# Kernel optimization log

Measured on AMD Instinct MI355X. Metric: run time of the kernel, lower is better.

Reference implementation:

```python
import jax, jax.numpy as jnp
import numpy as np

# dims: T tokens, H hidden, E experts, I expert intermediate, K top-k
T, H, E, I, K = 2048, 1024, 64, 768, 8


def setup_inputs() -> dict:
    key = jax.random.key(0)
    k0, k1, k2, k3, k4 = jax.random.split(key, 5)
    s = 0.02  # init scale
    return {
        "hidden_states": jax.random.normal(k0, (T, H), jnp.float32),
        "w_router": jax.random.normal(k1, (E, H), jnp.float32) * s,   # gate (router) Linear, no bias
        "w_gate": jax.random.normal(k2, (E, I, H), jnp.float32) * s,  # per-expert gate_proj (out,in)
        "w_up": jax.random.normal(k3, (E, I, H), jnp.float32) * s,    # per-expert up_proj
        "w_down": jax.random.normal(k4, (E, H, I), jnp.float32) * s,  # per-expert down_proj
    }


def reference(hidden_states, w_router, w_gate, w_up, w_down):
    x = hidden_states  # (T, H)
    # --- router: softmax scores, top-k selection, renormalize (select_experts, softmax scoring) ---
    router_logits = jnp.einsum("th,eh->te", x, w_router)          # (T, E)
    probs = jax.nn.softmax(router_logits, axis=-1)
    topk_w, topk_ids = jax.lax.top_k(probs, K)                     # (T, K)
    topk_w = topk_w / jnp.sum(topk_w, axis=-1, keepdims=True)      # renormalize=True
    # scatter per-slot weights into a (T, E) combine matrix (zero for unselected experts)
    route = jnp.zeros((x.shape[0], E), x.dtype)
    route = route.at[jnp.arange(x.shape[0])[:, None], topk_ids].add(topk_w)
    # --- experts: SwiGLU MLP per expert, weighted combine (FusedMoE dispatch/combine) ---
    g = jnp.einsum("th,eih->tei", x, w_gate)                       # (T, E, I)
    u = jnp.einsum("th,eih->tei", x, w_up)
    h = jax.nn.silu(g) * u
    y = jnp.einsum("tei,ehi,te->th", h, w_down, route)             # weighted scatter-combine
    return y
```

## Files before the change

### kernel.cpp

```cpp
#include <hip/hip_runtime.h>
#include <hip/hip_bf16.h>
#include <cstdint>
#include <cstddef>

#define T_TOK 2048
#define H_DIM 1024
#define E_NUM 64
#define I_DIM 768
#define K_TOP 8
#define BM 384

typedef __attribute__((ext_vector_type(8))) __bf16 bf16x8;
typedef __attribute__((ext_vector_type(4))) __bf16 bf16x4;
typedef __attribute__((ext_vector_type(8))) unsigned short u16x8;
typedef __attribute__((ext_vector_type(4))) float f32x4;
typedef unsigned short ushort_t;

__device__ __forceinline__ unsigned short f2bf(float f) {
  uint32_t u = __builtin_bit_cast(uint32_t, f);
  u += 0x7fffu + ((u >> 16) & 1u);
  return (unsigned short)(u >> 16);
}

__device__ __forceinline__ bf16x8 cvt8b(f32x4 a, f32x4 b) {
  bf16x8 r;
  r[0] = (__bf16)a[0]; r[1] = (__bf16)a[1]; r[2] = (__bf16)a[2]; r[3] = (__bf16)a[3];
  r[4] = (__bf16)b[0]; r[5] = (__bf16)b[1]; r[6] = (__bf16)b[2]; r[7] = (__bf16)b[3];
  return r;
}

__device__ __forceinline__ bf16x4 cvt4b(f32x4 a) {
  bf16x4 r;
  r[0] = (__bf16)a[0]; r[1] = (__bf16)a[1]; r[2] = (__bf16)a[2]; r[3] = (__bf16)a[3];
  return r;
}

__device__ __forceinline__ void async16(const void* l, const void* g) {
  __builtin_amdgcn_global_load_lds(
      (const __attribute__((address_space(1))) unsigned int*)g,
      (__attribute__((address_space(3))) unsigned int*)l, 16, 0, 0);
}

__global__ __launch_bounds__(256) void xcast_kernel(const float* __restrict__ x,
                                                    ushort_t* __restrict__ xb) {
  int i = blockIdx.x * 256 + threadIdx.x;
  const f32x4* s = (const f32x4*)(x + (size_t)i * 8);
  *(bf16x8*)(xb + (size_t)i * 8) = cvt8b(s[0], s[1]);
}

__global__ __launch_bounds__(64) void router_kernel(
    const float* __restrict__ x, const float* __restrict__ wr,
    int* __restrict__ topk_id, float* __restrict__ topk_w,
    int* __restrict__ counts) {
  const int t0 = blockIdx.x * 4;
  const int e = threadIdx.x;
  const float4* wv = (const float4*)(wr + (size_t)e * H_DIM);
  const float4* xv0 = (const float4*)(x + (size_t)t0 * H_DIM);
  const float4* xv1 = (const float4*)(x + (size_t)(t0 + 1) * H_DIM);
  const float4* xv2 = (const float4*)(x + (size_t)(t0 + 2) * H_DIM);
  const float4* xv3 = (const float4*)(x + (size_t)(t0 + 3) * H_DIM);
  float acc0 = 0.f, acc1 = 0.f, acc2 = 0.f, acc3 = 0.f;
#pragma unroll 4
  for (int i = 0; i < H_DIM / 4; ++i) {
    float4 b = wv[i];
    float4 a0 = xv0[i], a1 = xv1[i], a2 = xv2[i], a3 = xv3[i];
    acc0 = fmaf(a0.x, b.x, fmaf(a0.y, b.y, fmaf(a0.z, b.z, fmaf(a0.w, b.w, acc0))));
    acc1 = fmaf(a1.x, b.x, fmaf(a1.y, b.y, fmaf(a1.z, b.z, fmaf(a1.w, b.w, acc1))));
    acc2 = fmaf(a2.x, b.x, fmaf(a2.y, b.y, fmaf(a2.z, b.z, fmaf(a2.w, b.w, acc2))));
    acc3 = fmaf(a3.x, b.x, fmaf(a3.y, b.y, fmaf(a3.z, b.z, fmaf(a3.w, b.w, acc3))));
  }
  float accs[4] = {acc0, acc1, acc2, acc3};
#pragma unroll 1
  for (int tt = 0; tt < 4; ++tt) {
    int t = t0 + tt;
    float acc = accs[tt];
    float m = acc;
    for (int o = 32; o; o >>= 1) m = fmaxf(m, __shfl_xor(m, o));
    float p = __expf(acc - m);
    float s = p;
    for (int o = 32; o; o >>= 1) s += __shfl_xor(s, o);
    p /= s;
    float v = p;
    int sid = 0;
    float sw = 0.f;
    for (int k = 0; k < K_TOP; ++k) {
      float bv = v;
      int bi = e;
      for (int o = 32; o; o >>= 1) {
        float ov = __shfl_xor(bv, o);
        int oi = __shfl_xor(bi, o);
        if (ov > bv || (ov == bv && oi < bi)) { bv = ov; bi = oi; }
      }
      if (e == k) { sid = bi; sw = bv; }
      if (e == bi) v = -1.f;
    }
    float ssum = (e < K_TOP) ? sw : 0.f;
    for (int o = 32; o; o >>= 1) ssum += __shfl_xor(ssum, o);
    if (e < K_TOP) {
      topk_id[t * K_TOP + e] = sid;
      topk_w[t * K_TOP + e] = sw / ssum;
      atomicAdd(&counts[sid], 1);
    }
  }
}

__global__ __launch_bounds__(64) void scan_kernel(
    const int* __restrict__ counts, int* __restrict__ offsets,
    int* __restrict__ cursor) {
  int e = threadIdx.x;
  int ne = counts[e];
  int x = ne;
  for (int o = 1; o < 64; o <<= 1) {
    int v = __shfl_up(x, o);
    if (e >= o) x += v;
  }
  int excl = x - ne;
  offsets[e] = excl;
  cursor[e] = excl;
}

__global__ __launch_bounds__(256) void build_kernel(
    const int* __restrict__ topk_id, const float* __restrict__ topk_w,
    int* __restrict__ cursor, int* __restrict__ pair_token, float* __restrict__ pair_w) {
  int i = blockIdx.x * 256 + threadIdx.x;
  int t = i >> 3;
  int e = topk_id[i];
  int pos = atomicAdd(&cursor[e], 1);
  pair_token[pos] = t;
  pair_w[pos] = topk_w[i];
}


#define GU_NIT 32

__global__ __launch_bounds__(768, 3) void gemm_gu_kernel(
    const ushort_t* __restrict__ xb, const float* __restrict__ wg,
    const float* __restrict__ wu, const int* __restrict__ offsets,
    const int* __restrict__ counts, const int* __restrict__ pair_token,
    ushort_t* __restrict__ h_buf) {
  int idx = (blockIdx.x & 7) * 96 + (blockIdx.x >> 3);
  int e = idx / 12, nt = idx - e * 12;
  int ne = counts[e], off = offsets[e];
  int ib = nt * 64;

  __shared__ __align__(16) ushort_t Xs[2][BM * 32];
  __shared__ __align__(16) ushort_t Gs[2][64 * 32];
  __shared__ __align__(16) ushort_t Us[2][64 * 32];
  __shared__ int sTok[BM];

  const int tid = threadIdx.x;
  const int lane = tid & 63;
  const int wid = tid >> 6;
  if (tid < BM) {
    sTok[tid] = pair_token[off + (tid < ne ? tid : ne - 1)];
  }
  __syncthreads();

  const ushort_t* xsrc[2];
#pragma unroll
  for (int j = 0; j < 2; ++j) {
    int p = j * 768 + tid;
    int row = p >> 2, c = p & 3;
    xsrc[j] = xb + (size_t)sTok[row] * H_DIM + ((c ^ ((row >> 1) & 3)) << 3);
  }
  const float* gsrc = wg;
  const float* usrc = wu;
  int wdsti = 0;
  if (wid < 8) {
    int wrow = tid >> 3, wq = tid & 7;
    size_t ro = ((size_t)e * I_DIM + ib + wrow) * H_DIM + wq * 4;
    gsrc = wg + ro;
    usrc = wu + ro;
    wdsti = wrow * 32 + (((wq >> 1) ^ ((wrow >> 1) & 3)) << 3) + ((wq & 1) << 2);
  }

  const int wrM = wid >> 1, wrN = wid & 1;
  const int lrow = lane & 15, lk = lane >> 4;
  const bool wact = (wrM * 64) < ne;

  f32x4 accG[4][2], accU[4][2];
#pragma unroll
  for (int mi = 0; mi < 4; ++mi)
#pragma unroll
    for (int ni = 0; ni < 2; ++ni) {
      accG[mi][ni] = f32x4{0.f, 0.f, 0.f, 0.f};
      accU[mi][ni] = f32x4{0.f, 0.f, 0.f, 0.f};
    }

  f32x4 gA = {0, 0, 0, 0}, uA = {0, 0, 0, 0};

#define GU_XDMA(B, K0)                                             \
  do {                                                             \
    async16(&Xs[B][(wid * 64) * 8], xsrc[0] + (K0));               \
    async16(&Xs[B][(768 + wid * 64) * 8], xsrc[1] + (K0));         \
  } while (0)

  GU_XDMA(0, 0);
  if (wid < 8) {
    gA = *(const f32x4*)(gsrc);
    uA = *(const f32x4*)(usrc);
  }
  asm volatile("s_waitcnt vmcnt(0)" ::: "memory");
  __builtin_amdgcn_sched_barrier(0);
  if (wid < 8) {
    *(bf16x4*)&Gs[0][wdsti] = cvt4b(gA);
    *(bf16x4*)&Us[0][wdsti] = cvt4b(uA);
  }
  asm volatile("s_waitcnt lgkmcnt(0)" ::: "memory");
  __builtin_amdgcn_s_barrier();
  __builtin_amdgcn_sched_barrier(0);

#pragma unroll 2
  for (int K = 0; K < GU_NIT; ++K) {
    const int B = K & 1;
    if (K + 1 < GU_NIT) {
      GU_XDMA(B ^ 1, (K + 1) * 32);
      if (wid < 8) {
        gA = *(const f32x4*)(gsrc + (K + 1) * 32);
        uA = *(const f32x4*)(usrc + (K + 1) * 32);
      }
    }
    if (wact) {
      __builtin_amdgcn_s_setprio(1);
      bf16x8 af[4];
#pragma unroll
      for (int mi = 0; mi < 4; ++mi) {
        int r = wrM * 64 + mi * 16 + lrow;
        af[mi] = __builtin_bit_cast(
            bf16x8, *(const u16x8*)&Xs[B][r * 32 + ((lk ^ ((r >> 1) & 3)) << 3)]);
      }
#pragma unroll
      for (int ni = 0; ni < 2; ++ni) {
        int br = wrN * 32 + ni * 16 + lrow;
        int ci = br * 32 + ((lk ^ ((br >> 1) & 3)) << 3);
        bf16x8 bg = __builtin_bit_cast(bf16x8, *(const u16x8*)&Gs[B][ci]);
        bf16x8 bu = __builtin_bit_cast(bf16x8, *(const u16x8*)&Us[B][ci]);
#pragma unroll
        for (int mi = 0; mi < 4; ++mi) {
          accG[mi][ni] = __builtin_amdgcn_mfma_f32_16x16x32_bf16(af[mi], bg, accG[mi][ni], 0, 0, 0);
          accU[mi][ni] = __builtin_amdgcn_mfma_f32_16x16x32_bf16(af[mi], bu, accU[mi][ni], 0, 0, 0);
        }
      }
      __builtin_amdgcn_s_setprio(0);
    }
    asm volatile("s_waitcnt vmcnt(0)" ::: "memory");
    __builtin_amdgcn_sched_barrier(0);
    if (K + 1 < GU_NIT && wid < 8) {
      *(bf16x4*)&Gs[B ^ 1][wdsti] = cvt4b(gA);
      *(bf16x4*)&Us[B ^ 1][wdsti] = cvt4b(uA);
    }
    asm volatile("s_waitcnt lgkmcnt(0)" ::: "memory");
    __builtin_amdgcn_s_barrier();
    __builtin_amdgcn_sched_barrier(0);
  }
#undef GU_XDMA

#pragma unroll
  for (int mi = 0; mi < 4; ++mi)
#pragma unroll
    for (int ni = 0; ni < 2; ++ni)
#pragma unroll
      for (int r = 0; r < 4; ++r) {
        int grow = wrM * 64 + mi * 16 + lk * 4 + r;
        if (grow < ne) {
          int col = ib + wrN * 32 + ni * 16 + lrow;
          float g = accG[mi][ni][r], u = accU[mi][ni][r];
          float hv = g / (1.f + __expf(-g)) * u;
          h_buf[(size_t)(off + grow) * I_DIM + col] = f2bf(hv);
        }
      }
}

#define DN_NIT 24

__global__ __launch_bounds__(768, 3) void gemm_down_kernel(
    const ushort_t* __restrict__ h_buf, const float* __restrict__ wd,
    const int* __restrict__ offsets, const int* __restrict__ counts,
    const int* __restrict__ pair_token, const float* __restrict__ pair_w,
    float* __restrict__ y) {
  int idx = (blockIdx.x & 7) * 64 + (blockIdx.x >> 3);
  int e = idx >> 3, nt = idx & 7;
  int ne = counts[e], off = offsets[e];
  int hb = nt * 128;

  __shared__ __align__(16) ushort_t Ah[2][BM * 32];
  __shared__ __align__(16) ushort_t Bs[2][128 * 32];
  __shared__ int sTok[BM];
  __shared__ float sPw[BM];

  const int tid = threadIdx.x;
  const int lane = tid & 63;
  const int wid = tid >> 6;
  if (tid < BM) {
    int ix = off + (tid < ne ? tid : ne - 1);
    sTok[tid] = pair_token[ix];
    sPw[tid] = pair_w[ix];
  }
  __syncthreads();

  const ushort_t* asrc[2];
#pragma unroll
  for (int j = 0; j < 2; ++j) {
    int p = j * 768 + tid;
    int row = p >> 2, c = p & 3;
    int hr = off + (row < ne ? row : ne - 1);
    asrc[j] = h_buf + (size_t)hr * I_DIM + ((c ^ ((row >> 1) & 3)) << 3);
  }
  const float* bsrc0 = wd;
  const float* bsrc1 = wd;
  int bdst0 = 0, bdst1 = 0;
  if (wid < 8) {
    int r0 = tid >> 3, q0 = tid & 7;
    bsrc0 = wd + ((size_t)e * H_DIM + hb + r0) * I_DIM + q0 * 4;
    bdst0 = r0 * 32 + (((q0 >> 1) ^ ((r0 >> 1) & 3)) << 3) + ((q0 & 1) << 2);
    int p1 = 512 + tid;
    int r1 = p1 >> 3, q1 = p1 & 7;
    bsrc1 = wd + ((size_t)e * H_DIM + hb + r1) * I_DIM + q1 * 4;
    bdst1 = r1 * 32 + (((q1 >> 1) ^ ((r1 >> 1) & 3)) << 3) + ((q1 & 1) << 2);
  }

  const int wrM = wid >> 1, wrN = wid & 1;
  const int lrow = lane & 15, lk = lane >> 4;
  const bool wact = (wrM * 64) < ne;

  f32x4 acc[4][4];
#pragma unroll
  for (int mi = 0; mi < 4; ++mi)
#pragma unroll
    for (int ni = 0; ni < 4; ++ni) acc[mi][ni] = f32x4{0.f, 0.f, 0.f, 0.f};

  f32x4 bA = {0, 0, 0, 0}, bB = {0, 0, 0, 0};

#define DN_ADMA(B, K0)                                             \
  do {                                                             \
    async16(&Ah[B][(wid * 64) * 8], asrc[0] + (K0));               \
    async16(&Ah[B][(768 + wid * 64) * 8], asrc[1] + (K0));         \
  } while (0)

  DN_ADMA(0, 0);
  if (wid < 8) {
    bA = *(const f32x4*)(bsrc0);
    bB = *(const f32x4*)(bsrc1);
  }
  asm volatile("s_waitcnt vmcnt(0)" ::: "memory");
  __builtin_amdgcn_sched_barrier(0);
  if (wid < 8) {
    *(bf16x4*)&Bs[0][bdst0] = cvt4b(bA);
    *(bf16x4*)&Bs[0][bdst1] = cvt4b(bB);
  }
  asm volatile("s_waitcnt lgkmcnt(0)" ::: "memory");
  __builtin_amdgcn_s_barrier();
  __builtin_amdgcn_sched_barrier(0);

#pragma unroll 2
  for (int K = 0; K < DN_NIT; ++K) {
    const int B = K & 1;
    if (K + 1 < DN_NIT) {
      DN_ADMA(B ^ 1, (K + 1) * 32);
      if (wid < 8) {
        bA = *(const f32x4*)(bsrc0 + (K + 1) * 32);
        bB = *(const f32x4*)(bsrc1 + (K + 1) * 32);
      }
    }
    if (wact) {
      __builtin_amdgcn_s_setprio(1);
      bf16x8 af[4];
#pragma unroll
      for (int mi = 0; mi < 4; ++mi) {
        int r = wrM * 64 + mi * 16 + lrow;
        af[mi] = __builtin_bit_cast(
            bf16x8, *(const u16x8*)&Ah[B][r * 32 + ((lk ^ ((r >> 1) & 3)) << 3)]);
      }
#pragma unroll
      for (int ni = 0; ni < 4; ++ni) {
        int br = wrN * 64 + ni * 16 + lrow;
        bf16x8 bb = __builtin_bit_cast(
            bf16x8, *(const u16x8*)&Bs[B][br * 32 + ((lk ^ ((br >> 1) & 3)) << 3)]);
#pragma unroll
        for (int mi = 0; mi < 4; ++mi)
          acc[mi][ni] = __builtin_amdgcn_mfma_f32_16x16x32_bf16(af[mi], bb, acc[mi][ni], 0, 0, 0);
      }
      __builtin_amdgcn_s_setprio(0);
    }
    asm volatile("s_waitcnt vmcnt(0)" ::: "memory");
    __builtin_amdgcn_sched_barrier(0);
    if (K + 1 < DN_NIT && wid < 8) {
      *(bf16x4*)&Bs[B ^ 1][bdst0] = cvt4b(bA);
      *(bf16x4*)&Bs[B ^ 1][bdst1] = cvt4b(bB);
    }
    asm volatile("s_waitcnt lgkmcnt(0)" ::: "memory");
    __builtin_amdgcn_s_barrier();
    __builtin_amdgcn_sched_barrier(0);
  }
#undef DN_ADMA

#pragma unroll
  for (int mi = 0; mi < 4; ++mi)
#pragma unroll
    for (int ni = 0; ni < 4; ++ni)
#pragma unroll
      for (int r = 0; r < 4; ++r) {
        int grow = wrM * 64 + mi * 16 + lk * 4 + r;
        if (grow < ne) {
          int col = hb + wrN * 64 + ni * 16 + lrow;
          float val = acc[mi][ni][r] * sPw[grow];
          unsafeAtomicAdd(&y[(size_t)sTok[grow] * H_DIM + col], val);
        }
      }
}

extern "C" void kernel_launch(void* const* d_in, const int* in_sizes, int n_in,
                              void* d_out, int out_size, void* d_ws, size_t ws_size,
                              hipStream_t stream) {
  const float* x  = (const float*)d_in[0];
  const float* wr = (const float*)d_in[1];
  const float* wg = (const float*)d_in[2];
  const float* wu = (const float*)d_in[3];
  const float* wd = (const float*)d_in[4];
  float* y = (float*)d_out;

  char* ws = (char*)d_ws;
  int* counts    = (int*)(ws + 0);
  int* offsets   = (int*)(ws + 256);
  int* cursor    = (int*)(ws + 512);
  int*   topk_id    = (int*)(ws + 2048);
  float* topk_w     = (float*)(ws + 2048 + 1 * 65536);
  int*   pair_token = (int*)(ws + 2048 + 2 * 65536);
  float* pair_w     = (float*)(ws + 2048 + 3 * 65536);
  ushort_t* h_buf = (ushort_t*)(ws + 2048 + 4 * 65536);
  ushort_t* xb = (ushort_t*)(ws + 2048 + 4 * 65536 + (size_t)T_TOK * I_DIM * K_TOP * 2);

  hipMemsetAsync(counts, 0, 256, stream);
  hipMemsetAsync(y, 0, (size_t)T_TOK * H_DIM * sizeof(float), stream);

  xcast_kernel<<<(T_TOK * H_DIM / 8) / 256, 256, 0, stream>>>(x, xb);
  router_kernel<<<T_TOK / 4, 64, 0, stream>>>(x, wr, topk_id, topk_w, counts);
  scan_kernel<<<1, 64, 0, stream>>>(counts, offsets, cursor);
  build_kernel<<<(T_TOK * K_TOP) / 256, 256, 0, stream>>>(topk_id, topk_w, cursor, pair_token, pair_w);
  gemm_gu_kernel<<<768, 768, 0, stream>>>(
      xb, wg, wu, offsets, counts, pair_token, h_buf);
  gemm_down_kernel<<<512, 768, 0, stream>>>(
      h_buf, wd, offsets, counts, pair_token, pair_w, y);
}
```

Before: 372.7 us.

## Retile MoE GEMMs into 256-row expert tiles with a dynamic tile list

The scan kernel now builds a compact list of 256-row M tiles per expert, at most two per expert. Both expert GEMMs are launched over that list with XCD-aware index decoding, so blocks for empty tiles exit early. This replaces the fixed 384-row padded tiles, which wasted MFMA work and LDS. The gate/up kernel now uses 512-thread blocks that stack gate and up weights in one 256-row B tile, exchange the up accumulators through LDS for the SiLU epilogue, and use a four-phase software pipeline. The cost is extra barriers and LDS traffic in the epilogue, and any expert with more than 512 assigned tokens would be truncated.

Measured after the change: 556.9 us. 1.49x slower.

```diff
diff --git a/kernel.cpp b/kernel.cpp
--- a/kernel.cpp
+++ b/kernel.cpp
@@ -8,10 +8,8 @@
 #define E_NUM 64
 #define I_DIM 768
 #define K_TOP 8
-#define BM 384
 
 typedef __attribute__((ext_vector_type(8))) __bf16 bf16x8;
-typedef __attribute__((ext_vector_type(4))) __bf16 bf16x4;
 typedef __attribute__((ext_vector_type(8))) unsigned short u16x8;
 typedef __attribute__((ext_vector_type(4))) float f32x4;
 typedef unsigned short ushort_t;
@@ -22,17 +20,11 @@
   return (unsigned short)(u >> 16);
 }
 
-__device__ __forceinline__ bf16x8 cvt8b(f32x4 a, f32x4 b) {
+__device__ __forceinline__ u16x8 cvt8b(f32x4 a, f32x4 b) {
   bf16x8 r;
   r[0] = (__bf16)a[0]; r[1] = (__bf16)a[1]; r[2] = (__bf16)a[2]; r[3] = (__bf16)a[3];
   r[4] = (__bf16)b[0]; r[5] = (__bf16)b[1]; r[6] = (__bf16)b[2]; r[7] = (__bf16)b[3];
-  return r;
-}
-
-__device__ __forceinline__ bf16x4 cvt4b(f32x4 a) {
-  bf16x4 r;
-  r[0] = (__bf16)a[0]; r[1] = (__bf16)a[1]; r[2] = (__bf16)a[2]; r[3] = (__bf16)a[3];
-  return r;
+  return __builtin_bit_cast(u16x8, r);
 }
 
 __device__ __forceinline__ void async16(const void* l, const void* g) {
@@ -41,11 +33,19 @@
       (__attribute__((address_space(3))) unsigned int*)l, 16, 0, 0);
 }
 
+__device__ __forceinline__ int xcd_decode(int wg0, int n_act) {
+  int q = n_act >> 3, r = n_act & 7;
+  int xcd = wg0 & 7, rank = wg0 >> 3;
+  int cnt = q + (xcd < r ? 1 : 0);
+  if (rank >= cnt) return -1;
+  return (xcd < r ? xcd * (q + 1) : r * (q + 1) + (xcd - r) * q) + rank;
+}
+
 __global__ __launch_bounds__(256) void xcast_kernel(const float* __restrict__ x,
                                                     ushort_t* __restrict__ xb) {
   int i = blockIdx.x * 256 + threadIdx.x;
   const f32x4* s = (const f32x4*)(x + (size_t)i * 8);
-  *(bf16x8*)(xb + (size_t)i * 8) = cvt8b(s[0], s[1]);
+  *(u16x8*)(xb + (size_t)i * 8) = cvt8b(s[0], s[1]);
 }
 
 __global__ __launch_bounds__(64) void router_kernel(
@@ -106,7 +106,8 @@
 
 __global__ __launch_bounds__(64) void scan_kernel(
     const int* __restrict__ counts, int* __restrict__ offsets,
-    int* __restrict__ cursor) {
+    int* __restrict__ cursor, int* __restrict__ tile_list,
+    int* __restrict__ n_tiles) {
   int e = threadIdx.x;
   int ne = counts[e];
   int x = ne;
@@ -117,6 +118,16 @@
   int excl = x - ne;
   offsets[e] = excl;
   cursor[e] = excl;
+  int ntl = (ne + 255) >> 8;
+  if (ntl > 2) ntl = 2;
+  int y2 = ntl;
+  for (int o = 1; o < 64; o <<= 1) {
+    int v = __shfl_up(y2, o);
+    if (e >= o) y2 += v;
+  }
+  int texcl = y2 - ntl;
+  for (int m = 0; m < ntl; ++m) tile_list[texcl + m] = (e << 2) | m;
+  if (e == 63) *n_tiles = texcl + ntl;
 }
 
 __global__ __launch_bounds__(256) void build_kernel(
@@ -133,276 +144,343 @@
 
 #define GU_NIT 32
 
-__global__ __launch_bounds__(768, 3) void gemm_gu_kernel(
+__global__ __launch_bounds__(512, 2) void gemm_gu_kernel(
     const ushort_t* __restrict__ xb, const float* __restrict__ wg,
     const float* __restrict__ wu, const int* __restrict__ offsets,
     const int* __restrict__ counts, const int* __restrict__ pair_token,
+    const int* __restrict__ tile_list, const int* __restrict__ n_tiles,
     ushort_t* __restrict__ h_buf) {
-  int idx = (blockIdx.x & 7) * 96 + (blockIdx.x >> 3);
-  int e = idx / 12, nt = idx - e * 12;
+  int idx = xcd_decode(blockIdx.x, (*n_tiles) * 6);
+  if (idx < 0) return;
+  int tl = idx / 6, nt = idx - tl * 6;
+  int ent = tile_list[tl];
+  int e = ent >> 2, mt = ent & 3;
   int ne = counts[e], off = offsets[e];
-  int ib = nt * 64;
-
-  __shared__ __align__(16) ushort_t Xs[2][BM * 32];
-  __shared__ __align__(16) ushort_t Gs[2][64 * 32];
-  __shared__ __align__(16) ushort_t Us[2][64 * 32];
-  __shared__ int sTok[BM];
+  int ib = nt * 128;
+  int vr = ne - mt * 256;
+  if (vr <= 0) return;
+  if (vr > 256) vr = 256;
+
+  __shared__ __align__(16) char L[66560];
+  ushort_t* AsB = (ushort_t*)L;
+  ushort_t* BlB = (ushort_t*)(L + 32768);
+  int* sTok = (int*)(L + 65536);
 
   const int tid = threadIdx.x;
   const int lane = tid & 63;
   const int wid = tid >> 6;
-  if (tid < BM) {
-    sTok[tid] = pair_token[off + (tid < ne ? tid : ne - 1)];
+  const int wrM = wid >> 2, wrN = wid & 3;
+  const int lrow = lane & 15, lk = lane >> 4;
+
+  if (tid < 256) {
+    int p = mt * 256 + tid;
+    sTok[tid] = pair_token[off + (p < ne ? p : ne - 1)];
   }
   __syncthreads();
 
   const ushort_t* xsrc[2];
+  int adst[2];
 #pragma unroll
   for (int j = 0; j < 2; ++j) {
-    int p = j * 768 + tid;
+    int p = j * 512 + tid;
     int row = p >> 2, c = p & 3;
     xsrc[j] = xb + (size_t)sTok[row] * H_DIM + ((c ^ ((row >> 1) & 3)) << 3);
-  }
-  const float* gsrc = wg;
-  const float* usrc = wu;
-  int wdsti = 0;
-  if (wid < 8) {
-    int wrow = tid >> 3, wq = tid & 7;
-    size_t ro = ((size_t)e * I_DIM + ib + wrow) * H_DIM + wq * 4;
-    gsrc = wg + ro;
-    usrc = wu + ro;
-    wdsti = wrow * 32 + (((wq >> 1) ^ ((wrow >> 1) & 3)) << 3) + ((wq & 1) << 2);
-  }
-
-  const int wrM = wid >> 1, wrN = wid & 1;
-  const int lrow = lane & 15, lk = lane >> 4;
-  const bool wact = (wrM * 64) < ne;
-
-  f32x4 accG[4][2], accU[4][2];
-#pragma unroll
-  for (int mi = 0; mi < 4; ++mi)
-#pragma unroll
-    for (int ni = 0; ni < 2; ++ni) {
-      accG[mi][ni] = f32x4{0.f, 0.f, 0.f, 0.f};
-      accU[mi][ni] = f32x4{0.f, 0.f, 0.f, 0.f};
+    adst[j] = (j * 512 + wid * 64) * 8;
+  }
+  const int brow = tid >> 1;
+  const int cs0 = (tid & 1) * 2, cs1 = cs0 + 1;
+  const float* bq = (brow < 128)
+      ? wg + ((size_t)e * I_DIM + ib + brow) * H_DIM
+      : wu + ((size_t)e * I_DIM + ib + brow - 128) * H_DIM;
+  const float* bsrc0 = bq + cs0 * 8;
+  const float* bsrc1 = bq + cs1 * 8;
+  const int bd0 = (brow * 4 + (cs0 ^ ((brow >> 1) & 3))) * 8;
+  const int bd1 = (brow * 4 + (cs1 ^ ((brow >> 1) & 3))) * 8;
+
+  const bool wact = (wrM * 128) < vr;
+
+  f32x4 acc[8][4];
+#pragma unroll
+  for (int mi = 0; mi < 8; ++mi)
+#pragma unroll
+    for (int ni = 0; ni < 4; ++ni) acc[mi][ni] = f32x4{0.f, 0.f, 0.f, 0.f};
+
+#define GU_ADMA(NB, K0)                                           \
+  do {                                                            \
+    async16(&AsB[(NB) * 8192 + adst[0]], xsrc[0] + (K0));         \
+    async16(&AsB[(NB) * 8192 + adst[1]], xsrc[1] + (K0));         \
+  } while (0)
+
+#define GU_AF(AB, MI)                                                        \
+  do {                                                                       \
+    int R0 = wrM * 128 + (MI) * 16 + lrow;                                   \
+    int R1 = R0 + 16;                                                        \
+    af0 = *(const u16x8*)&AsB[(AB) * 8192 + R0 * 32 + ((lk ^ ((R0 >> 1) & 3)) << 3)]; \
+    af1 = *(const u16x8*)&AsB[(AB) * 8192 + R1 * 32 + ((lk ^ ((R1 >> 1) & 3)) << 3)]; \
+  } while (0)
+
+#define GU_MFMA2(MI)                                                         \
+  _Pragma("unroll") for (int ni = 0; ni < 4; ++ni) {                         \
+    acc[MI][ni] = __builtin_amdgcn_mfma_f32_16x16x32_bf16(                   \
+        __builtin_bit_cast(bf16x8, af0), __builtin_bit_cast(bf16x8, bf[ni]), \
+        acc[MI][ni], 0, 0, 0);                                               \
+    acc[(MI) + 1][ni] = __builtin_amdgcn_mfma_f32_16x16x32_bf16(             \
+        __builtin_bit_cast(bf16x8, af1), __builtin_bit_cast(bf16x8, bf[ni]), \
+        acc[(MI) + 1][ni], 0, 0, 0);                                         \
+  }
+
+#define FENCE_LGKM                                             \
+  asm volatile("s_waitcnt lgkmcnt(0)" ::: "memory");           \
+  __builtin_amdgcn_sched_barrier(0)
+
+  GU_ADMA(0, 0);
+  {
+    f32x4 p0 = *(const f32x4*)(bsrc0), p1 = *(const f32x4*)(bsrc0 + 4);
+    f32x4 p2 = *(const f32x4*)(bsrc1), p3 = *(const f32x4*)(bsrc1 + 4);
+    *(u16x8*)&BlB[bd0] = cvt8b(p0, p1);
+    *(u16x8*)&BlB[bd1] = cvt8b(p2, p3);
+  }
+  FENCE_LGKM;
+  __builtin_amdgcn_s_barrier();
+
+#pragma unroll 1
+  for (int t = 0; t < GU_NIT; ++t) {
+    const int b = t & 1, nb = b ^ 1;
+    const int kn = (t + 1 < GU_NIT) ? (t + 1) * 32 : 0;
+    u16x8 bf[4], af0, af1;
+    f32x4 br0, br1, br2, br3;
+    br0 = *(const f32x4*)(bsrc0 + kn);
+    br1 = *(const f32x4*)(bsrc0 + kn + 4);
+    asm volatile("s_waitcnt vmcnt(2)" ::: "memory");
+    __builtin_amdgcn_sched_barrier(0);
+    __builtin_amdgcn_s_barrier();
+    if (wact) {
+#pragma unroll
+      for (int ni = 0; ni < 4; ++ni) {
+        int Rb = wrN * 64 + ni * 16 + lrow;
+        bf[ni] = *(const u16x8*)&BlB[b * 8192 + Rb * 32 + ((lk ^ ((Rb >> 1) & 3)) << 3)];
+      }
+      GU_AF(b, 0);
     }
-
-  f32x4 gA = {0, 0, 0, 0}, uA = {0, 0, 0, 0};
-
-#define GU_XDMA(B, K0)                                             \
-  do {                                                             \
-    async16(&Xs[B][(wid * 64) * 8], xsrc[0] + (K0));               \
-    async16(&Xs[B][(768 + wid * 64) * 8], xsrc[1] + (K0));         \
-  } while (0)
-
-  GU_XDMA(0, 0);
-  if (wid < 8) {
-    gA = *(const f32x4*)(gsrc);
-    uA = *(const f32x4*)(usrc);
-  }
-  asm volatile("s_waitcnt vmcnt(0)" ::: "memory");
-  __builtin_amdgcn_sched_barrier(0);
-  if (wid < 8) {
-    *(bf16x4*)&Gs[0][wdsti] = cvt4b(gA);
-    *(bf16x4*)&Us[0][wdsti] = cvt4b(uA);
-  }
-  asm volatile("s_waitcnt lgkmcnt(0)" ::: "memory");
-  __builtin_amdgcn_s_barrier();
-  __builtin_amdgcn_sched_barrier(0);
-
-#pragma unroll 2
-  for (int K = 0; K < GU_NIT; ++K) {
-    const int B = K & 1;
-    if (K + 1 < GU_NIT) {
-      GU_XDMA(B ^ 1, (K + 1) * 32);
-      if (wid < 8) {
-        gA = *(const f32x4*)(gsrc + (K + 1) * 32);
-        uA = *(const f32x4*)(usrc + (K + 1) * 32);
-      }
+    FENCE_LGKM;
+    __builtin_amdgcn_s_setprio(1);
+    if (wact) { GU_MFMA2(0); }
+    __builtin_amdgcn_s_setprio(0);
+    __builtin_amdgcn_s_barrier();
+    br2 = *(const f32x4*)(bsrc1 + kn);
+    br3 = *(const f32x4*)(bsrc1 + kn + 4);
+    if (wact) GU_AF(b, 2);
+    FENCE_LGKM;
+    __builtin_amdgcn_s_setprio(1);
+    if (wact) { GU_MFMA2(2); }
+    __builtin_amdgcn_s_setprio(0);
+    __builtin_amdgcn_s_barrier();
+    GU_ADMA(nb, kn);
+    if (wact) GU_AF(b, 4);
+    FENCE_LGKM;
+    __builtin_amdgcn_s_setprio(1);
+    if (wact) { GU_MFMA2(4); }
+    __builtin_amdgcn_s_setprio(0);
+    __builtin_amdgcn_s_barrier();
+    *(u16x8*)&BlB[nb * 8192 + bd0] = cvt8b(br0, br1);
+    *(u16x8*)&BlB[nb * 8192 + bd1] = cvt8b(br2, br3);
+    if (wact) GU_AF(b, 6);
+    FENCE_LGKM;
+    __builtin_amdgcn_s_setprio(1);
+    if (wact) { GU_MFMA2(6); }
+    __builtin_amdgcn_s_setprio(0);
+    __builtin_amdgcn_s_barrier();
+  }
+#undef GU_ADMA
+#undef GU_AF
+#undef GU_MFMA2
+
+  float* ex = (float*)L;
+#pragma unroll 1
+  for (int rnd = 0; rnd < 2; ++rnd) {
+    if (wrN == 2 + rnd) {
+#pragma unroll
+      for (int mi = 0; mi < 8; ++mi)
+#pragma unroll
+        for (int ni = 0; ni < 4; ++ni)
+#pragma unroll
+          for (int r = 0; r < 4; ++r)
+            ex[(wrM * 128 + mi * 16 + lk * 4 + r) * 64 + ni * 16 + lrow] = acc[mi][ni][r];
     }
-    if (wact) {
-      __builtin_amdgcn_s_setprio(1);
-      bf16x8 af[4];
-#pragma unroll
-      for (int mi = 0; mi < 4; ++mi) {
-        int r = wrM * 64 + mi * 16 + lrow;
-        af[mi] = __builtin_bit_cast(
-            bf16x8, *(const u16x8*)&Xs[B][r * 32 + ((lk ^ ((r >> 1) & 3)) << 3)]);
-      }
-#pragma unroll
-      for (int ni = 0; ni < 2; ++ni) {
-        int br = wrN * 32 + ni * 16 + lrow;
-        int ci = br * 32 + ((lk ^ ((br >> 1) & 3)) << 3);
-        bf16x8 bg = __builtin_bit_cast(bf16x8, *(const u16x8*)&Gs[B][ci]);
-        bf16x8 bu = __builtin_bit_cast(bf16x8, *(const u16x8*)&Us[B][ci]);
-#pragma unroll
-        for (int mi = 0; mi < 4; ++mi) {
-          accG[mi][ni] = __builtin_amdgcn_mfma_f32_16x16x32_bf16(af[mi], bg, accG[mi][ni], 0, 0, 0);
-          accU[mi][ni] = __builtin_amdgcn_mfma_f32_16x16x32_bf16(af[mi], bu, accU[mi][ni], 0, 0, 0);
-        }
-      }
-      __builtin_amdgcn_s_setprio(0);
+    __syncthreads();
+    if (wrN == rnd) {
+#pragma unroll
+      for (int mi = 0; mi < 8; ++mi)
+#pragma unroll
+        for (int ni = 0; ni < 4; ++ni)
+#pragma unroll
+          for (int r = 0; r < 4; ++r) {
+            int grow = wrM * 128 + mi * 16 + lk * 4 + r;
+            if (grow < vr) {
+              float g = acc[mi][ni][r];
+              float u = ex[grow * 64 + ni * 16 + lrow];
+              float hv = g / (1.f + __expf(-g)) * u;
+              int col = ib + rnd * 64 + ni * 16 + lrow;
+              h_buf[(size_t)(off + mt * 256 + grow) * I_DIM + col] = f2bf(hv);
+            }
+          }
     }
-    asm volatile("s_waitcnt vmcnt(0)" ::: "memory");
-    __builtin_amdgcn_sched_barrier(0);
-    if (K + 1 < GU_NIT && wid < 8) {
-      *(bf16x4*)&Gs[B ^ 1][wdsti] = cvt4b(gA);
-      *(bf16x4*)&Us[B ^ 1][wdsti] = cvt4b(uA);
-    }
-    asm volatile("s_waitcnt lgkmcnt(0)" ::: "memory");
-    __builtin_amdgcn_s_barrier();
-    __builtin_amdgcn_sched_barrier(0);
-  }
-#undef GU_XDMA
-
-#pragma unroll
-  for (int mi = 0; mi < 4; ++mi)
-#pragma unroll
-    for (int ni = 0; ni < 2; ++ni)
-#pragma unroll
-      for (int r = 0; r < 4; ++r) {
-        int grow = wrM * 64 + mi * 16 + lk * 4 + r;
-        if (grow < ne) {
-          int col = ib + wrN * 32 + ni * 16 + lrow;
-          float g = accG[mi][ni][r], u = accU[mi][ni][r];
-          float hv = g / (1.f + __expf(-g)) * u;
-          h_buf[(size_t)(off + grow) * I_DIM + col] = f2bf(hv);
-        }
-      }
+    __syncthreads();
+  }
 }
 
 #define DN_NIT 24
 
-__global__ __launch_bounds__(768, 3) void gemm_down_kernel(
+__global__ __launch_bounds__(512, 4) void gemm_down_kernel(
     const ushort_t* __restrict__ h_buf, const float* __restrict__ wd,
     const int* __restrict__ offsets, const int* __restrict__ counts,
     const int* __restrict__ pair_token, const float* __restrict__ pair_w,
+    const int* __restrict__ tile_list, const int* __restrict__ n_tiles,
     float* __restrict__ y) {
-  int idx = (blockIdx.x & 7) * 64 + (blockIdx.x >> 3);
-  int e = idx >> 3, nt = idx & 7;
+  int idx = xcd_decode(blockIdx.x, (*n_tiles) * 8);
+  if (idx < 0) return;
+  int tl = idx >> 3, nt = idx & 7;
+  int ent = tile_list[tl];
+  int e = ent >> 2, mt = ent & 3;
   int ne = counts[e], off = offsets[e];
   int hb = nt * 128;
-
-  __shared__ __align__(16) ushort_t Ah[2][BM * 32];
-  __shared__ __align__(16) ushort_t Bs[2][128 * 32];
-  __shared__ int sTok[BM];
-  __shared__ float sPw[BM];
+  int vr = ne - mt * 256;
+  if (vr <= 0) return;
+  if (vr > 256) vr = 256;
+
+  __shared__ __align__(16) char L[51200];
+  ushort_t* AsB = (ushort_t*)L;
+  ushort_t* BlB = (ushort_t*)(L + 32768);
+  int* sTok = (int*)(L + 49152);
+  float* sPw = (float*)(L + 50176);
 
   const int tid = threadIdx.x;
   const int lane = tid & 63;
   const int wid = tid >> 6;
-  if (tid < BM) {
-    int ix = off + (tid < ne ? tid : ne - 1);
+  const int wrM = wid >> 2, wrN = wid & 3;
+  const int lrow = lane & 15, lk = lane >> 4;
+
+  if (tid < 256) {
+    int p = mt * 256 + tid;
+    int ix = off + (p < ne ? p : ne - 1);
     sTok[tid] = pair_token[ix];
     sPw[tid] = pair_w[ix];
   }
   __syncthreads();
 
   const ushort_t* asrc[2];
+  int adst[2];
 #pragma unroll
   for (int j = 0; j < 2; ++j) {
-    int p = j * 768 + tid;
+    int p = j * 512 + tid;
     int row = p >> 2, c = p & 3;
-    int hr = off + (row < ne ? row : ne - 1);
+    int pr = mt * 256 + row;
+    int hr = off + (pr < ne ? pr : ne - 1);
     asrc[j] = h_buf + (size_t)hr * I_DIM + ((c ^ ((row >> 1) & 3)) << 3);
-  }
-  const float* bsrc0 = wd;
-  const float* bsrc1 = wd;
-  int bdst0 = 0, bdst1 = 0;
-  if (wid < 8) {
-    int r0 = tid >> 3, q0 = tid & 7;
-    bsrc0 = wd + ((size_t)e * H_DIM + hb + r0) * I_DIM + q0 * 4;
-    bdst0 = r0 * 32 + (((q0 >> 1) ^ ((r0 >> 1) & 3)) << 3) + ((q0 & 1) << 2);
-    int p1 = 512 + tid;
-    int r1 = p1 >> 3, q1 = p1 & 7;
-    bsrc1 = wd + ((size_t)e * H_DIM + hb + r1) * I_DIM + q1 * 4;
-    bdst1 = r1 * 32 + (((q1 >> 1) ^ ((r1 >> 1) & 3)) << 3) + ((q1 & 1) << 2);
-  }
-
-  const int wrM = wid >> 1, wrN = wid & 1;
-  const int lrow = lane & 15, lk = lane >> 4;
-  const bool wact = (wrM * 64) < ne;
-
-  f32x4 acc[4][4];
-#pragma unroll
-  for (int mi = 0; mi < 4; ++mi)
-#pragma unroll
-    for (int ni = 0; ni < 4; ++ni) acc[mi][ni] = f32x4{0.f, 0.f, 0.f, 0.f};
-
-  f32x4 bA = {0, 0, 0, 0}, bB = {0, 0, 0, 0};
-
-#define DN_ADMA(B, K0)                                             \
-  do {                                                             \
-    async16(&Ah[B][(wid * 64) * 8], asrc[0] + (K0));               \
-    async16(&Ah[B][(768 + wid * 64) * 8], asrc[1] + (K0));         \
+    adst[j] = (j * 512 + wid * 64) * 8;
+  }
+  const int brow = tid >> 2, csl = tid & 3;
+  const float* bsrc = wd + ((size_t)e * H_DIM + hb + brow) * I_DIM + ((csl ^ 0) * 8);
+  const int bd = (brow * 4 + (csl ^ ((brow >> 1) & 3))) * 8;
+
+  const bool wact = (wrM * 128) < vr;
+
+  f32x4 acc[8][2];
+#pragma unroll
+  for (int mi = 0; mi < 8; ++mi)
+#pragma unroll
+    for (int ni = 0; ni < 2; ++ni) acc[mi][ni] = f32x4{0.f, 0.f, 0.f, 0.f};
+
+#define DN_ADMA(NB, K0)                                           \
+  do {                                                            \
+    async16(&AsB[(NB) * 8192 + adst[0]], asrc[0] + (K0));         \
+    async16(&AsB[(NB) * 8192 + adst[1]], asrc[1] + (K0));         \
   } while (0)
 
+#define DN_AF(AB, MI)                                                        \
+  do {                                                                       \
+    int R0 = wrM * 128 + (MI) * 16 + lrow;                                   \
+    int R1 = R0 + 16;                                                        \
+    af0 = *(const u16x8*)&AsB[(AB) * 8192 + R0 * 32 + ((lk ^ ((R0 >> 1) & 3)) << 3)]; \
+    af1 = *(const u16x8*)&AsB[(AB) * 8192 + R1 * 32 + ((lk ^ ((R1 >> 1) & 3)) << 3)]; \
+  } while (0)
+
+#define DN_MFMA2(MI)                                                         \
+  _Pragma("unroll") for (int ni = 0; ni < 2; ++ni) {                         \
+    acc[MI][ni] = __builtin_amdgcn_mfma_f32_16x16x32_bf16(                   \
+        __builtin_bit_cast(bf16x8, af0), __builtin_bit_cast(bf16x8, bf[ni]), \
+        acc[MI][ni], 0, 0, 0);                                               \
+    acc[(MI) + 1][ni] = __builtin_amdgcn_mfma_f32_16x16x32_bf16(             \
+        __builtin_bit_cast(bf16x8, af1), __builtin_bit_cast(bf16x8, bf[ni]), \
+        acc[(MI) + 1][ni], 0, 0, 0);                                         \
+  }
+
   DN_ADMA(0, 0);
-  if (wid < 8) {
-    bA = *(const f32x4*)(bsrc0);
-    bB = *(const f32x4*)(bsrc1);
-  }
-  asm volatile("s_waitcnt vmcnt(0)" ::: "memory");
-  __builtin_amdgcn_sched_barrier(0);
-  if (wid < 8) {
-    *(bf16x4*)&Bs[0][bdst0] = cvt4b(bA);
-    *(bf16x4*)&Bs[0][bdst1] = cvt4b(bB);
-  }
-  asm volatile("s_waitcnt lgkmcnt(0)" ::: "memory");
+  {
+    f32x4 p0 = *(const f32x4*)(bsrc), p1 = *(const f32x4*)(bsrc + 4);
+    *(u16x8*)&BlB[bd] = cvt8b(p0, p1);
+  }
+  FENCE_LGKM;
   __builtin_amdgcn_s_barrier();
-  __builtin_amdgcn_sched_barrier(0);
-
-#pragma unroll 2
-  for (int K = 0; K < DN_NIT; ++K) {
-    const int B = K & 1;
-    if (K + 1 < DN_NIT) {
-      DN_ADMA(B ^ 1, (K + 1) * 32);
-      if (wid < 8) {
-        bA = *(const f32x4*)(bsrc0 + (K + 1) * 32);
-        bB = *(const f32x4*)(bsrc1 + (K + 1) * 32);
+
+#pragma unroll 1
+  for (int t = 0; t < DN_NIT; ++t) {
+    const int b = t & 1, nb = b ^ 1;
+    const int kn = (t + 1 < DN_NIT) ? (t + 1) * 32 : 0;
+    u16x8 bf[2], af0, af1;
+    f32x4 br0, br1;
+    br0 = *(const f32x4*)(bsrc + kn);
+    br1 = *(const f32x4*)(bsrc + kn + 4);
+    asm volatile("s_waitcnt vmcnt(2)" ::: "memory");
+    __builtin_amdgcn_sched_barrier(0);
+    __builtin_amdgcn_s_barrier();
+    if (wact) {
+#pragma unroll
+      for (int ni = 0; ni < 2; ++ni) {
+        int Rb = wrN * 32 + ni * 16 + lrow;
+        bf[ni] = *(const u16x8*)&BlB[b * 4096 + Rb * 32 + ((lk ^ ((Rb >> 1) & 3)) << 3)];
       }
+      DN_AF(b, 0);
     }
-    if (wact) {
-      __builtin_amdgcn_s_setprio(1);
-      bf16x8 af[4];
-#pragma unroll
-      for (int mi = 0; mi < 4; ++mi) {
-        int r = wrM * 64 + mi * 16 + lrow;
-        af[mi] = __builtin_bit_cast(
-            bf16x8, *(const u16x8*)&Ah[B][r * 32 + ((lk ^ ((r >> 1) & 3)) << 3)]);
-      }
-#pragma unroll
-      for (int ni = 0; ni < 4; ++ni) {
-        int br = wrN * 64 + ni * 16 + lrow;
-        bf16x8 bb = __builtin_bit_cast(
-            bf16x8, *(const u16x8*)&Bs[B][br * 32 + ((lk ^ ((br >> 1) & 3)) << 3)]);
-#pragma unroll
-        for (int mi = 0; mi < 4; ++mi)
-          acc[mi][ni] = __builtin_amdgcn_mfma_f32_16x16x32_bf16(af[mi], bb, acc[mi][ni], 0, 0, 0);
-      }
-      __builtin_amdgcn_s_setprio(0);
-    }
-    asm volatile("s_waitcnt vmcnt(0)" ::: "memory");
-    __builtin_amdgcn_sched_barrier(0);
-    if (K + 1 < DN_NIT && wid < 8) {
-      *(bf16x4*)&Bs[B ^ 1][bdst0] = cvt4b(bA);
-      *(bf16x4*)&Bs[B ^ 1][bdst1] = cvt4b(bB);
-    }
-    asm volatile("s_waitcnt lgkmcnt(0)" ::: "memory");
-    __builtin_amdgcn_s_barrier();
-    __builtin_amdgcn_sched_barrier(0);
+    FENCE_LGKM;
+    __builtin_amdgcn_s_setprio(1);
+    if (wact) { DN_MFMA2(0); }
+    __builtin_amdgcn_s_setprio(0);
+    __builtin_amdgcn_s_barrier();
+    if (wact) DN_AF(b, 2);
+    FENCE_LGKM;
+    __builtin_amdgcn_s_setprio(1);
+    if (wact) { DN_MFMA2(2); }
+    __builtin_amdgcn_s_setprio(0);
+    __builtin_amdgcn_s_barrier();
+    DN_ADMA(nb, kn);
+    if (wact) DN_AF(b, 4);
+    FENCE_LGKM;
+    __builtin_amdgcn_s_setprio(1);
+    if (wact) { DN_MFMA2(4); }
+    __builtin_amdgcn_s_setprio(0);
+    __builtin_amdgcn_s_barrier();
+    *(u16x8*)&BlB[nb * 4096 + bd] = cvt8b(br0, br1);
+    if (wact) DN_AF(b, 6);
+    FENCE_LGKM;
+    __builtin_amdgcn_s_setprio(1);
+    if (wact) { DN_MFMA2(6); }
+    __builtin_amdgcn_s_setprio(0);
+    __builtin_amdgcn_s_barrier();
   }
 #undef DN_ADMA
-
-#pragma unroll
-  for (int mi = 0; mi < 4; ++mi)
-#pragma unroll
-    for (int ni = 0; ni < 4; ++ni)
+#undef DN_AF
+#undef DN_MFMA2
+
+#pragma unroll
+  for (int mi = 0; mi < 8; ++mi)
+#pragma unroll
+    for (int ni = 0; ni < 2; ++ni)
 #pragma unroll
       for (int r = 0; r < 4; ++r) {
-        int grow = wrM * 64 + mi * 16 + lk * 4 + r;
-        if (grow < ne) {
-          int col = hb + wrN * 64 + ni * 16 + lrow;
+        int grow = wrM * 128 + mi * 16 + lk * 4 + r;
+        if (grow < vr) {
+          int col = hb + wrN * 32 + ni * 16 + lrow;
           float val = acc[mi][ni][r] * sPw[grow];
           unsafeAtomicAdd(&y[(size_t)sTok[grow] * H_DIM + col], val);
         }
@@ -423,6 +501,8 @@
   int* counts    = (int*)(ws + 0);
   int* offsets   = (int*)(ws + 256);
   int* cursor    = (int*)(ws + 512);
+  int* n_tiles   = (int*)(ws + 768);
+  int* tile_list = (int*)(ws + 1024);
   int*   topk_id    = (int*)(ws + 2048);
   float* topk_w     = (float*)(ws + 2048 + 1 * 65536);
   int*   pair_token = (int*)(ws + 2048 + 2 * 65536);
@@ -435,10 +515,10 @@
 
   xcast_kernel<<<(T_TOK * H_DIM / 8) / 256, 256, 0, stream>>>(x, xb);
   router_kernel<<<T_TOK / 4, 64, 0, stream>>>(x, wr, topk_id, topk_w, counts);
-  scan_kernel<<<1, 64, 0, stream>>>(counts, offsets, cursor);
+  scan_kernel<<<1, 64, 0, stream>>>(counts, offsets, cursor, tile_list, n_tiles);
   build_kernel<<<(T_TOK * K_TOP) / 256, 256, 0, stream>>>(topk_id, topk_w, cursor, pair_token, pair_w);
-  gemm_gu_kernel<<<768, 768, 0, stream>>>(
-      xb, wg, wu, offsets, counts, pair_token, h_buf);
-  gemm_down_kernel<<<512, 768, 0, stream>>>(
-      h_buf, wd, offsets, counts, pair_token, pair_w, y);
-}
+  gemm_gu_kernel<<<128 * 6, 512, 0, stream>>>(
+      xb, wg, wu, offsets, counts, pair_token, tile_list, n_tiles, h_buf);
+  gemm_down_kernel<<<128 * 8, 512, 0, stream>>>(
+      h_buf, wd, offsets, counts, pair_token, pair_w, tile_list, n_tiles, y);
+}
```
